# Kernel optimization log

Hardware: AMD Instinct MI355X
Metric: run time of the kernel (lower is better)

## Reference

```python
import jax, jax.numpy as jnp
import numpy as np
from jax import lax

B, N, T, H, E, D, K = 2, 1024, 4096, 256, 2, 2, 9


def angle2vector(a):
    return jnp.stack([jnp.sin(a), jnp.cos(a)], axis=-1)


def setup_inputs() -> dict:
    key = jax.random.key(0)
    ks = jax.random.split(key, 16)
    s = jnp.float32(0.05)
    return {
        "x": jax.random.normal(ks[0], (B, N, T), jnp.float32),
        "z": jax.random.uniform(ks[1], (B, T, E, D), jnp.float32, 0.0, 2.0 * np.pi),
        # encoder: depthwise conv (groups=N) then two 1x1 convs
        "dw_w": jax.random.normal(ks[2], (N, 1, K), jnp.float32) * s,
        "dw_b": jax.random.normal(ks[3], (N,), jnp.float32) * s,
        "w1": jax.random.normal(ks[4], (H, N), jnp.float32) * s,
        "b1": jax.random.normal(ks[5], (H,), jnp.float32) * s,
        "w2": jax.random.normal(ks[6], (H, H), jnp.float32) * s,
        "b2": jax.random.normal(ks[7], (H,), jnp.float32) * s,
        # heads (1x1 convs)
        "wm": jax.random.normal(ks[8], (E * D * 2, H), jnp.float32) * s,
        "bm": jax.random.normal(ks[9], (E * D * 2,), jnp.float32) * s,
        "wv": jax.random.normal(ks[10], (E * D, H), jnp.float32) * s,
        "bv": jax.random.normal(ks[11], (E * D,), jnp.float32) * s,
        # feature basis / readout params
        "receptive_fields": jax.random.uniform(ks[12], (N, E, D), jnp.float32, 0.0, 2.0 * np.pi),
        "ensemble_weights": jax.random.normal(ks[13], (N, E), jnp.float32),
        "final_scale": jax.random.normal(ks[14], (N,), jnp.float32) * s,
        "log_tuning_width": jnp.full((1,), np.log(2.0), jnp.float32),
    }


def reference(x, z, dw_w, dw_b, w1, b1, w2, b2, wm, bm, wv, bv,
              receptive_fields, ensemble_weights, final_scale, log_tuning_width):
    # ---- encoder ----
    # depthwise conv1d, kernel_size=K, padding='same', groups=N
    h = lax.conv_general_dilated(
        x, dw_w, window_strides=(1,), padding="SAME",
        feature_group_count=N, dimension_numbers=("NCH", "OIH", "NCH"))
    h = h + dw_b[None, :, None]
    h = jax.nn.relu(jnp.einsum("hn,bnt->bht", w1, h) + b1[None, :, None])
    h = jax.nn.relu(jnp.einsum("gh,bht->bgt", w2, h) + b2[None, :, None])

    # ---- heads ----
    mu = jnp.einsum("oh,bht->bot", wm, h) + bm[None, :, None]  # [B, E*D*2, T]
    mu = mu.transpose(0, 2, 1).reshape(B, T, E, D, 2)
    logvar = jnp.einsum("oh,bht->bot", wv, h) + bv[None, :, None]  # [B, E*D, T]
    logvar = logvar.transpose(0, 2, 1).reshape(B, T, E, D)
    # normalize encodings onto unit circle
    mu = mu / jnp.sqrt(jnp.sum(mu ** 2, axis=-1, keepdims=True))

    # ---- feature basis ('bump') ----
    zv = angle2vector(z)                     # [B, T, E, D, 2]
    rfv = angle2vector(receptive_fields)     # [N, E, D, 2]
    diff = zv[:, :, None] - rfv[None, None]  # [B, T, N, E, D, 2]
    dist = jnp.sum(diff ** 2, axis=(4, 5))   # [B, T, N, E]
    response = jnp.exp(-dist / jnp.exp(log_tuning_width))  # nonlinearity='exp'

    # ---- ensemble-weighted readout ----
    ew = jax.nn.softmax(ensemble_weights, axis=1)  # [N, E]
    responses = jnp.einsum("btne,ne->btn", response, ew)
    responses = responses * jnp.exp(final_scale)[None, None]
    responses = responses.transpose(0, 2, 1)  # [B, N, T]
    return responses, z, mu, logvar
```

## Files before the change

### kernel.cpp

```cpp
#include <hip/hip_runtime.h>
#include <hip/hip_bf16.h>

#define B_ 2
#define N_ 1024
#define T_ 4096
#define H_ 256
#define ROWS_ 8192

typedef float f32x4 __attribute__((ext_vector_type(4)));
typedef __bf16 bf16x8 __attribute__((ext_vector_type(8)));

__device__ __forceinline__ void gl16(const void* g, void* l) {
  __builtin_amdgcn_global_load_lds(
      (const __attribute__((address_space(1))) void*)g,
      (__attribute__((address_space(3))) void*)l, 16, 0, 0);
}

#define WAITV(N) asm volatile("s_waitcnt vmcnt(" #N ")" ::: "memory")
#define FENCE_ALL() asm volatile("s_waitcnt vmcnt(0) lgkmcnt(0)" ::: "memory")
#define LGKM0() asm volatile("s_waitcnt lgkmcnt(0)" ::: "memory")

__global__ __launch_bounds__(256) void cvt_pack(
    const float* __restrict__ w1, const float* __restrict__ w2,
    __bf16* __restrict__ w1p, __bf16* __restrict__ w2p) {
  const int i = blockIdx.x * 256 + threadIdx.x;
  const float* src;
  __bf16* dst;
  int K, kt, s;
  if (i < 65536) {
    kt = i >> 11; s = i & 2047; src = w1; K = 1024; dst = w1p + (size_t)i * 8;
  } else {
    int j = i - 65536;
    kt = j >> 11; s = j & 2047; src = w2; K = 256; dst = w2p + (size_t)j * 8;
  }
  const int pl = s >> 10;
  const int idx = s & 1023;
  const int g = idx >> 2;
  const int cc = (idx & 3) ^ ((g >> 1) & 3);
  const float* p = src + (size_t)g * K + kt * 32 + cc * 8;
  bf16x8 o;
  #pragma unroll
  for (int e = 0; e < 8; ++e) {
    float v = p[e];
    __bf16 h = (__bf16)v;
    o[e] = pl ? (__bf16)(v - (float)h) : h;
  }
  *(bf16x8*)dst = o;
}

__global__ __launch_bounds__(256) void dwconv_t(
    const float* __restrict__ x, const float* __restrict__ w,
    const float* __restrict__ bias, __bf16* __restrict__ h0h,
    __bf16* __restrict__ h0l) {
  __shared__ float xs[64][76];
  const int tid = threadIdx.x;
  const int t0 = blockIdx.x * 64;
  const int n0 = blockIdx.y * 64;
  const int b = blockIdx.z;
  for (int i = tid; i < 64 * 72; i += 256) {
    int rr = i / 72, cc = i % 72;
    int tt = t0 - 4 + cc;
    xs[rr][cc] = (tt >= 0 && tt < T_) ? x[((size_t)(b * N_ + n0 + rr)) * T_ + tt] : 0.f;
  }
  const int nl = tid & 63;
  const int tg = tid >> 6;
  float wr[9];
  #pragma unroll
  for (int k = 0; k < 9; ++k) wr[k] = w[(n0 + nl) * 9 + k];
  const float bb = bias[n0 + nl];
  __syncthreads();
  float win[24];
  #pragma unroll
  for (int c = 0; c < 6; ++c)
    *(f32x4*)&win[c * 4] = *(const f32x4*)&xs[nl][tg * 16 + c * 4];
  const size_t obase = ((size_t)b * T_ + t0 + tg * 16) * N_ + n0 + nl;
  #pragma unroll
  for (int j = 0; j < 16; ++j) {
    float acc = bb;
    #pragma unroll
    for (int k = 0; k < 9; ++k) acc = fmaf(win[j + k], wr[k], acc);
    __bf16 h = (__bf16)acc;
    h0h[obase + (size_t)j * N_] = h;
    h0l[obase + (size_t)j * N_] = (__bf16)(acc - (float)h);
  }
}

__global__ __launch_bounds__(512) void encoder_fused(
    const __bf16* __restrict__ Ah, const __bf16* __restrict__ Al,
    const __bf16* __restrict__ W1P, const float* __restrict__ b1,
    const __bf16* __restrict__ W2P, const float* __restrict__ b2,
    const float* __restrict__ wm, const float* __restrict__ bm,
    const float* __restrict__ wv, const float* __restrict__ bv,
    float* __restrict__ out_mu, float* __restrict__ out_lv) {
  __shared__ __attribute__((aligned(16))) char smem[126976];
  char* const ASB = smem;
  char* const WSB = smem + 8192;
  char* const H1B = smem + 73728;
  float* const WMV = (float*)(smem + 106496);
  float* const H2S = (float*)(smem + 8192);

  const int tid = threadIdx.x;
  const int row0 = blockIdx.x * 32;
  const int lane = tid & 63;
  const int wid = tid >> 6;
  const int wt = (wid >> 2) * 16;
  const int wg = (wid & 3) * 64;
  const int lr = lane & 15;
  const int ls = lane >> 4;

  if (tid < 256) {
    #pragma unroll
    for (int i = 0; i < 8; ++i) WMV[tid * 20 + i] = wm[i * 256 + tid];
    #pragma unroll
    for (int i = 0; i < 4; ++i) WMV[tid * 20 + 8 + i] = wv[i * 256 + tid];
  }
  float b1g[4], b2g[4];
  #pragma unroll
  for (int ni = 0; ni < 4; ++ni) {
    b1g[ni] = b1[wg + ni * 16 + lr];
    b2g[ni] = b2[wg + ni * 16 + lr];
  }
  FENCE_ALL();

  const int a_pl = tid >> 7;
  const int a_idx = tid & 127;
  const int a_r = a_idx >> 2;
  const int a_c = (a_idx & 3) ^ ((a_r >> 1) & 3);
  const __bf16* a_src = (a_pl ? Al : Ah) + (size_t)(row0 + a_r) * 1024 + a_c * 8;
  char* const a_dst = ASB + a_pl * 2048 + a_idx * 16;

  auto STAGE_A = [&](int buf, int kt) {
    if (tid < 256) gl16(a_src + kt * 32, a_dst + buf * 4096);
  };
  auto STAGE_W = [&](int buf, int kt, const __bf16* WP) {
    const char* src = (const char*)WP + (size_t)kt * 32768 + tid * 16;
    char* dst = WSB + buf * 32768 + tid * 16;
    #pragma unroll
    for (int j = 0; j < 4; ++j) gl16(src + j * 8192, dst + j * 8192);
  };
  auto FR_A = [&](int cur, int pl, int r) {
    return *(const bf16x8*)(ASB + cur * 4096 + pl * 2048 + r * 64 +
                            (ls ^ ((r >> 1) & 3)) * 16);
  };
  auto FR_W = [&](int cur, int pl, int g) {
    return *(const bf16x8*)(WSB + cur * 32768 + pl * 16384 + g * 64 +
                            (ls ^ ((g >> 1) & 3)) * 16);
  };

  f32x4 acc[4];
  #pragma unroll
  for (int i = 0; i < 4; ++i) acc[i] = (f32x4)0.f;

  STAGE_A(0, 0); STAGE_W(0, 0, W1P);
  STAGE_A(1, 1); STAGE_W(1, 1, W1P);
  for (int kt = 0; kt < 32; ++kt) {
    const int cur = kt & 1;
    if (kt < 31) {
      if (tid < 256) WAITV(5); else WAITV(4);
    } else {
      WAITV(0);
    }
    __builtin_amdgcn_s_barrier();
    {
      const int ra = wt + lr;
      bf16x8 ah = FR_A(cur, 0, ra);
      bf16x8 al = FR_A(cur, 1, ra);
      __builtin_amdgcn_s_setprio(1);
      #pragma unroll
      for (int ni = 0; ni < 4; ++ni) {
        const int rw = wg + ni * 16 + lr;
        bf16x8 wh = FR_W(cur, 0, rw);
        bf16x8 wl = FR_W(cur, 1, rw);
        acc[ni] = __builtin_amdgcn_mfma_f32_16x16x32_bf16(ah, wh, acc[ni], 0, 0, 0);
        acc[ni] = __builtin_amdgcn_mfma_f32_16x16x32_bf16(ah, wl, acc[ni], 0, 0, 0);
        acc[ni] = __builtin_amdgcn_mfma_f32_16x16x32_bf16(al, wh, acc[ni], 0, 0, 0);
      }
      __builtin_amdgcn_s_setprio(0);
    }
    LGKM0();
    __builtin_amdgcn_s_barrier();
    if (kt < 30) { STAGE_A(cur, kt + 2); STAGE_W(cur, kt + 2, W1P); }
  }

  #pragma unroll
  for (int ni = 0; ni < 4; ++ni) {
    const int g = wg + ni * 16 + lr;
    const int c = g >> 3;
    #pragma unroll
    for (int reg = 0; reg < 4; ++reg) {
      const int t = wt + ls * 4 + reg;
      float v = fmaxf(acc[ni][reg] + b1g[ni], 0.f);
      __bf16 h = (__bf16)v;
      const int off = t * 512 + ((c ^ (t & 7)) * 16) + (g & 7) * 2;
      *(__bf16*)(H1B + off) = h;
      *(__bf16*)(H1B + 16384 + off) = (__bf16)(v - (float)h);
    }
    acc[ni] = (f32x4)0.f;
  }

  STAGE_W(0, 0, W2P);
  STAGE_W(1, 1, W2P);
  for (int kt = 0; kt < 8; ++kt) {
    const int cur = kt & 1;
    if (kt < 7) WAITV(4); else WAITV(0);
    LGKM0();
    __builtin_amdgcn_s_barrier();
    {
      const int t = wt + lr;
      const int ca = ((kt * 4 + ls) ^ (t & 7)) * 16;
      bf16x8 ah = *(const bf16x8*)(H1B + t * 512 + ca);
      bf16x8 al = *(const bf16x8*)(H1B + 16384 + t * 512 + ca);
      __builtin_amdgcn_s_setprio(1);
      #pragma unroll
      for (int ni = 0; ni < 4; ++ni) {
        const int rw = wg + ni * 16 + lr;
        bf16x8 wh = FR_W(cur, 0, rw);
        bf16x8 wl = FR_W(cur, 1, rw);
        acc[ni] = __builtin_amdgcn_mfma_f32_16x16x32_bf16(ah, wh, acc[ni], 0, 0, 0);
        acc[ni] = __builtin_amdgcn_mfma_f32_16x16x32_bf16(ah, wl, acc[ni], 0, 0, 0);
        acc[ni] = __builtin_amdgcn_mfma_f32_16x16x32_bf16(al, wh, acc[ni], 0, 0, 0);
      }
      __builtin_amdgcn_s_setprio(0);
    }
    LGKM0();
    __builtin_amdgcn_s_barrier();
    if (kt < 6) STAGE_W(cur, kt + 2, W2P);
  }

  #pragma unroll
  for (int ni = 0; ni < 4; ++ni) {
    const int g = wg + ni * 16 + lr;
    #pragma unroll
    for (int reg = 0; reg < 4; ++reg) {
      const int t = wt + ls * 4 + reg;
      H2S[t * 264 + g] = fmaxf(acc[ni][reg] + b2g[ni], 0.f);
    }
  }
  LGKM0();
  __builtin_amdgcn_s_barrier();

  const int ht = tid >> 4;
  const int sub = tid & 15;
  float s[12];
  #pragma unroll
  for (int o = 0; o < 12; ++o) s[o] = 0.f;
  #pragma unroll
  for (int j = 0; j < 16; ++j) {
    const int k = sub + j * 16;
    const float hv = H2S[ht * 264 + k];
    const float* wp = &WMV[k * 20];
    #pragma unroll
    for (int o = 0; o < 12; ++o) s[o] = fmaf(wp[o], hv, s[o]);
  }
  #pragma unroll
  for (int o = 0; o < 12; ++o) {
    s[o] += __shfl_xor(s[o], 1);
    s[o] += __shfl_xor(s[o], 2);
    s[o] += __shfl_xor(s[o], 4);
    s[o] += __shfl_xor(s[o], 8);
  }
  const size_t row = row0 + ht;
  if (sub == 0) {
    float mm[8];
    #pragma unroll
    for (int ed = 0; ed < 4; ++ed) {
      float m0 = s[ed * 2] + bm[ed * 2];
      float m1 = s[ed * 2 + 1] + bm[ed * 2 + 1];
      float inv = 1.f / sqrtf(m0 * m0 + m1 * m1);
      mm[ed * 2] = m0 * inv;
      mm[ed * 2 + 1] = m1 * inv;
    }
    *(float4*)&out_mu[row * 8] = make_float4(mm[0], mm[1], mm[2], mm[3]);
    *(float4*)&out_mu[row * 8 + 4] = make_float4(mm[4], mm[5], mm[6], mm[7]);
  } else if (sub == 1) {
    *(float4*)&out_lv[row * 4] =
        make_float4(s[8] + bv[0], s[9] + bv[1], s[10] + bv[2], s[11] + bv[3]);
  }
}

__global__ __launch_bounds__(256) void resp_kernel(
    const float* __restrict__ z, const float* __restrict__ rf,
    const float* __restrict__ ew, const float* __restrict__ fs,
    const float* __restrict__ ltw, float* __restrict__ out,
    float* __restrict__ out_z) {
  __shared__ float s_sin[32][4], s_cos[32][4], s_w[32][2];
  const int tid = threadIdx.x;
  const int tc = blockIdx.x;
  const int nc = blockIdx.y;
  const int b = blockIdx.z;
  if (tid < 128) {
    int nl = tid >> 2, ed = tid & 3;
    float a = rf[(nc * 32 + nl) * 4 + ed];
    s_sin[nl][ed] = sinf(a);
    s_cos[nl][ed] = cosf(a);
  }
  if (tid < 32) {
    int n = nc * 32 + tid;
    float e0 = ew[n * 2], e1 = ew[n * 2 + 1];
    float m = fmaxf(e0, e1);
    float x0 = expf(e0 - m), x1 = expf(e1 - m);
    float sc = expf(fs[n]) / (x0 + x1);
    s_w[tid][0] = x0 * sc;
    s_w[tid][1] = x1 * sc;
  }
  __syncthreads();
  const int t = tc * 1024 + (tid >> 6) * 256 + (tid & 63) * 4;
  const float inv_tw = expf(-ltw[0]);
  float sz[16], cz[16];
  #pragma unroll
  for (int j = 0; j < 4; ++j) {
    float4 zv = *(const float4*)&z[((size_t)b * T_ + t + j) * 4];
    if (nc == 0) *(float4*)&out_z[((size_t)b * T_ + t + j) * 4] = zv;
    sz[j * 4 + 0] = sinf(zv.x); cz[j * 4 + 0] = cosf(zv.x);
    sz[j * 4 + 1] = sinf(zv.y); cz[j * 4 + 1] = cosf(zv.y);
    sz[j * 4 + 2] = sinf(zv.z); cz[j * 4 + 2] = cosf(zv.z);
    sz[j * 4 + 3] = sinf(zv.w); cz[j * 4 + 3] = cosf(zv.w);
  }
  float* op = out + (size_t)b * N_ * T_ + (size_t)(nc * 32) * T_ + t;
  for (int nl = 0; nl < 32; ++nl) {
    const float ss0 = s_sin[nl][0], sc0 = s_cos[nl][0];
    const float ss1 = s_sin[nl][1], sc1 = s_cos[nl][1];
    const float ss2 = s_sin[nl][2], sc2 = s_cos[nl][2];
    const float ss3 = s_sin[nl][3], sc3 = s_cos[nl][3];
    const float w0 = s_w[nl][0], w1 = s_w[nl][1];
    float o[4];
    #pragma unroll
    for (int j = 0; j < 4; ++j) {
      float d0 = sz[j * 4] * ss0 + cz[j * 4] * sc0 + sz[j * 4 + 1] * ss1 + cz[j * 4 + 1] * sc1;
      float d1 = sz[j * 4 + 2] * ss2 + cz[j * 4 + 2] * sc2 + sz[j * 4 + 3] * ss3 + cz[j * 4 + 3] * sc3;
      float r0 = __expf((2.f * d0 - 4.f) * inv_tw);
      float r1 = __expf((2.f * d1 - 4.f) * inv_tw);
      o[j] = w0 * r0 + w1 * r1;
    }
    *(float4*)&op[(size_t)nl * T_] = make_float4(o[0], o[1], o[2], o[3]);
  }
}

extern "C" void kernel_launch(void* const* d_in, const int* in_sizes, int n_in,
                              void* d_out, int out_size, void* d_ws, size_t ws_size,
                              hipStream_t stream) {
  const float* x   = (const float*)d_in[0];
  const float* z   = (const float*)d_in[1];
  const float* dww = (const float*)d_in[2];
  const float* dwb = (const float*)d_in[3];
  const float* w1  = (const float*)d_in[4];
  const float* b1  = (const float*)d_in[5];
  const float* w2  = (const float*)d_in[6];
  const float* b2  = (const float*)d_in[7];
  const float* wm  = (const float*)d_in[8];
  const float* bm  = (const float*)d_in[9];
  const float* wv  = (const float*)d_in[10];
  const float* bv  = (const float*)d_in[11];
  const float* rf  = (const float*)d_in[12];
  const float* ew  = (const float*)d_in[13];
  const float* fs  = (const float*)d_in[14];
  const float* ltw = (const float*)d_in[15];

  float* out = (float*)d_out;
  float* out_resp = out;
  float* out_z    = out + (size_t)B_ * N_ * T_;
  float* out_mu   = out_z + (size_t)B_ * T_ * 4;
  float* out_lv   = out_mu + (size_t)B_ * T_ * 8;

  __bf16* h0h = (__bf16*)out_resp;
  __bf16* h0l = h0h + (size_t)ROWS_ * N_;

  __bf16* p = (__bf16*)d_ws;
  __bf16* w1p = p; p += 524288;
  __bf16* w2p = p; p += 131072;

  cvt_pack<<<320, 256, 0, stream>>>(w1, w2, w1p, w2p);
  dwconv_t<<<dim3(T_ / 64, N_ / 64, B_), 256, 0, stream>>>(x, dww, dwb, h0h, h0l);
  encoder_fused<<<dim3(ROWS_ / 32), 512, 0, stream>>>(
      h0h, h0l, w1p, b1, w2p, b2, wm, bm, wv, bv, out_mu, out_lv);
  resp_kernel<<<dim3(4, 32, 2), 256, 0, stream>>>(
      z, rf, ew, fs, ltw, out_resp, out_z);
}
```

Measured before the change: 175.8 us.

## Merge encoder and response kernels into one launch with larger row tiles

Fuses the encoder GEMM kernel and the response kernel into one launch: the first 128 blocks run the encoder, the remaining 128 blocks compute responses. Each encoder block now handles 64 rows, doubling the reuse of the staged weights, and the bf16 intermediate moves from the response output buffer into workspace so both parts can run at the same time. In exchange, shared memory per block grows and the encoder has fewer blocks to spread across the CUs.

```diff
diff --git a/kernel.cpp b/kernel.cpp
--- a/kernel.cpp
+++ b/kernel.cpp
@@ -6,6 +6,7 @@
 #define T_ 4096
 #define H_ 256
 #define ROWS_ 8192
+#define ENC_BLOCKS 128
 
 typedef float f32x4 __attribute__((ext_vector_type(4)));
 typedef __bf16 bf16x8 __attribute__((ext_vector_type(8)));
@@ -85,34 +86,96 @@
   }
 }
 
-__global__ __launch_bounds__(512) void encoder_fused(
+__global__ __launch_bounds__(512) void mega_kernel(
     const __bf16* __restrict__ Ah, const __bf16* __restrict__ Al,
     const __bf16* __restrict__ W1P, const float* __restrict__ b1,
     const __bf16* __restrict__ W2P, const float* __restrict__ b2,
     const float* __restrict__ wm, const float* __restrict__ bm,
     const float* __restrict__ wv, const float* __restrict__ bv,
-    float* __restrict__ out_mu, float* __restrict__ out_lv) {
-  __shared__ __attribute__((aligned(16))) char smem[126976];
+    float* __restrict__ out_mu, float* __restrict__ out_lv,
+    const float* __restrict__ z, const float* __restrict__ rf,
+    const float* __restrict__ ew, const float* __restrict__ fs,
+    const float* __restrict__ ltw, float* __restrict__ out_resp,
+    float* __restrict__ out_z) {
+  __shared__ __attribute__((aligned(16))) char smem[159744];
+  const int tid = threadIdx.x;
+
+  if (blockIdx.x >= ENC_BLOCKS) {
+    float* s_sin = (float*)smem;
+    float* s_cos = (float*)(smem + 512);
+    float* s_w   = (float*)(smem + 1024);
+    const int bid2 = blockIdx.x - ENC_BLOCKS;
+    const int nc = bid2 & 31;
+    const int tc = (bid2 >> 5) & 1;
+    const int b = bid2 >> 6;
+    if (tid < 128) {
+      int nl = tid >> 2, ed = tid & 3;
+      float a = rf[(nc * 32 + nl) * 4 + ed];
+      s_sin[nl * 4 + ed] = sinf(a);
+      s_cos[nl * 4 + ed] = cosf(a);
+    }
+    if (tid < 32) {
+      int n = nc * 32 + tid;
+      float e0 = ew[n * 2], e1 = ew[n * 2 + 1];
+      float m = fmaxf(e0, e1);
+      float x0 = expf(e0 - m), x1 = expf(e1 - m);
+      float sc = expf(fs[n]) / (x0 + x1);
+      s_w[tid * 2 + 0] = x0 * sc;
+      s_w[tid * 2 + 1] = x1 * sc;
+    }
+    __syncthreads();
+    const int t = tc * 2048 + tid * 4;
+    const float inv_tw = expf(-ltw[0]);
+    float sz[16], cz[16];
+    #pragma unroll
+    for (int j = 0; j < 4; ++j) {
+      float4 zv = *(const float4*)&z[((size_t)b * T_ + t + j) * 4];
+      if (nc == 0) *(float4*)&out_z[((size_t)b * T_ + t + j) * 4] = zv;
+      sz[j * 4 + 0] = sinf(zv.x); cz[j * 4 + 0] = cosf(zv.x);
+      sz[j * 4 + 1] = sinf(zv.y); cz[j * 4 + 1] = cosf(zv.y);
+      sz[j * 4 + 2] = sinf(zv.z); cz[j * 4 + 2] = cosf(zv.z);
+      sz[j * 4 + 3] = sinf(zv.w); cz[j * 4 + 3] = cosf(zv.w);
+    }
+    float* op = out_resp + (size_t)b * N_ * T_ + (size_t)(nc * 32) * T_ + t;
+    for (int nl = 0; nl < 32; ++nl) {
+      const float ss0 = s_sin[nl * 4 + 0], sc0 = s_cos[nl * 4 + 0];
+      const float ss1 = s_sin[nl * 4 + 1], sc1 = s_cos[nl * 4 + 1];
+      const float ss2 = s_sin[nl * 4 + 2], sc2 = s_cos[nl * 4 + 2];
+      const float ss3 = s_sin[nl * 4 + 3], sc3 = s_cos[nl * 4 + 3];
+      const float w0 = s_w[nl * 2 + 0], w1 = s_w[nl * 2 + 1];
+      float o[4];
+      #pragma unroll
+      for (int j = 0; j < 4; ++j) {
+        float d0 = sz[j * 4] * ss0 + cz[j * 4] * sc0 + sz[j * 4 + 1] * ss1 + cz[j * 4 + 1] * sc1;
+        float d1 = sz[j * 4 + 2] * ss2 + cz[j * 4 + 2] * sc2 + sz[j * 4 + 3] * ss3 + cz[j * 4 + 3] * sc3;
+        float r0 = __expf((2.f * d0 - 4.f) * inv_tw);
+        float r1 = __expf((2.f * d1 - 4.f) * inv_tw);
+        o[j] = w0 * r0 + w1 * r1;
+      }
+      *(float4*)&op[(size_t)nl * T_] = make_float4(o[0], o[1], o[2], o[3]);
+    }
+    return;
+  }
+
   char* const ASB = smem;
-  char* const WSB = smem + 8192;
-  char* const H1B = smem + 73728;
-  float* const WMV = (float*)(smem + 106496);
-  float* const H2S = (float*)(smem + 8192);
-
-  const int tid = threadIdx.x;
-  const int row0 = blockIdx.x * 32;
+  char* const WSB = smem + 16384;
+  char* const H1B = smem + 81920;
+  float* const WMV = (float*)(smem + 147456);
+  float* const H2S = (float*)smem;
+
+  const int row0 = blockIdx.x * 64;
   const int lane = tid & 63;
   const int wid = tid >> 6;
-  const int wt = (wid >> 2) * 16;
+  const int wt = (wid >> 2) * 32;
   const int wg = (wid & 3) * 64;
   const int lr = lane & 15;
   const int ls = lane >> 4;
 
   if (tid < 256) {
     #pragma unroll
-    for (int i = 0; i < 8; ++i) WMV[tid * 20 + i] = wm[i * 256 + tid];
-    #pragma unroll
-    for (int i = 0; i < 4; ++i) WMV[tid * 20 + 8 + i] = wv[i * 256 + tid];
+    for (int i = 0; i < 8; ++i) WMV[tid * 12 + i] = wm[i * 256 + tid];
+    #pragma unroll
+    for (int i = 0; i < 4; ++i) WMV[tid * 12 + 8 + i] = wv[i * 256 + tid];
   }
   float b1g[4], b2g[4];
   #pragma unroll
@@ -122,15 +185,15 @@
   }
   FENCE_ALL();
 
-  const int a_pl = tid >> 7;
-  const int a_idx = tid & 127;
+  const int a_pl = tid >> 8;
+  const int a_idx = tid & 255;
   const int a_r = a_idx >> 2;
   const int a_c = (a_idx & 3) ^ ((a_r >> 1) & 3);
   const __bf16* a_src = (a_pl ? Al : Ah) + (size_t)(row0 + a_r) * 1024 + a_c * 8;
-  char* const a_dst = ASB + a_pl * 2048 + a_idx * 16;
+  char* const a_dst = ASB + a_pl * 4096 + a_idx * 16;
 
   auto STAGE_A = [&](int buf, int kt) {
-    if (tid < 256) gl16(a_src + kt * 32, a_dst + buf * 4096);
+    gl16(a_src + kt * 32, a_dst + buf * 8192);
   };
   auto STAGE_W = [&](int buf, int kt, const __bf16* WP) {
     const char* src = (const char*)WP + (size_t)kt * 32768 + tid * 16;
@@ -139,7 +202,7 @@
     for (int j = 0; j < 4; ++j) gl16(src + j * 8192, dst + j * 8192);
   };
   auto FR_A = [&](int cur, int pl, int r) {
-    return *(const bf16x8*)(ASB + cur * 4096 + pl * 2048 + r * 64 +
+    return *(const bf16x8*)(ASB + cur * 8192 + pl * 4096 + r * 64 +
                             (ls ^ ((r >> 1) & 3)) * 16);
   };
   auto FR_W = [&](int cur, int pl, int g) {
@@ -147,33 +210,37 @@
                             (ls ^ ((g >> 1) & 3)) * 16);
   };
 
-  f32x4 acc[4];
-  #pragma unroll
-  for (int i = 0; i < 4; ++i) acc[i] = (f32x4)0.f;
+  f32x4 acc[2][4];
+  #pragma unroll
+  for (int i = 0; i < 2; ++i)
+    #pragma unroll
+    for (int j = 0; j < 4; ++j) acc[i][j] = (f32x4)0.f;
 
   STAGE_A(0, 0); STAGE_W(0, 0, W1P);
   STAGE_A(1, 1); STAGE_W(1, 1, W1P);
   for (int kt = 0; kt < 32; ++kt) {
     const int cur = kt & 1;
-    if (kt < 31) {
-      if (tid < 256) WAITV(5); else WAITV(4);
-    } else {
-      WAITV(0);
-    }
+    if (kt < 31) WAITV(5); else WAITV(0);
     __builtin_amdgcn_s_barrier();
     {
-      const int ra = wt + lr;
-      bf16x8 ah = FR_A(cur, 0, ra);
-      bf16x8 al = FR_A(cur, 1, ra);
+      bf16x8 ah[2], al[2];
+      #pragma unroll
+      for (int mi = 0; mi < 2; ++mi) {
+        ah[mi] = FR_A(cur, 0, wt + mi * 16 + lr);
+        al[mi] = FR_A(cur, 1, wt + mi * 16 + lr);
+      }
       __builtin_amdgcn_s_setprio(1);
       #pragma unroll
       for (int ni = 0; ni < 4; ++ni) {
         const int rw = wg + ni * 16 + lr;
         bf16x8 wh = FR_W(cur, 0, rw);
         bf16x8 wl = FR_W(cur, 1, rw);
-        acc[ni] = __builtin_amdgcn_mfma_f32_16x16x32_bf16(ah, wh, acc[ni], 0, 0, 0);
-        acc[ni] = __builtin_amdgcn_mfma_f32_16x16x32_bf16(ah, wl, acc[ni], 0, 0, 0);
-        acc[ni] = __builtin_amdgcn_mfma_f32_16x16x32_bf16(al, wh, acc[ni], 0, 0, 0);
+        #pragma unroll
+        for (int mi = 0; mi < 2; ++mi) {
+          acc[mi][ni] = __builtin_amdgcn_mfma_f32_16x16x32_bf16(ah[mi], wh, acc[mi][ni], 0, 0, 0);
+          acc[mi][ni] = __builtin_amdgcn_mfma_f32_16x16x32_bf16(ah[mi], wl, acc[mi][ni], 0, 0, 0);
+          acc[mi][ni] = __builtin_amdgcn_mfma_f32_16x16x32_bf16(al[mi], wh, acc[mi][ni], 0, 0, 0);
+        }
       }
       __builtin_amdgcn_s_setprio(0);
     }
@@ -183,20 +250,22 @@
   }
 
   #pragma unroll
-  for (int ni = 0; ni < 4; ++ni) {
-    const int g = wg + ni * 16 + lr;
-    const int c = g >> 3;
-    #pragma unroll
-    for (int reg = 0; reg < 4; ++reg) {
-      const int t = wt + ls * 4 + reg;
-      float v = fmaxf(acc[ni][reg] + b1g[ni], 0.f);
-      __bf16 h = (__bf16)v;
-      const int off = t * 512 + ((c ^ (t & 7)) * 16) + (g & 7) * 2;
-      *(__bf16*)(H1B + off) = h;
-      *(__bf16*)(H1B + 16384 + off) = (__bf16)(v - (float)h);
-    }
-    acc[ni] = (f32x4)0.f;
-  }
+  for (int mi = 0; mi < 2; ++mi)
+    #pragma unroll
+    for (int ni = 0; ni < 4; ++ni) {
+      const int g = wg + ni * 16 + lr;
+      const int c = g >> 3;
+      #pragma unroll
+      for (int reg = 0; reg < 4; ++reg) {
+        const int t = wt + mi * 16 + ls * 4 + reg;
+        float v = fmaxf(acc[mi][ni][reg] + b1g[ni], 0.f);
+        __bf16 h = (__bf16)v;
+        const int off = t * 512 + ((c ^ (t & 7)) * 16) + (g & 7) * 2;
+        *(__bf16*)(H1B + off) = h;
+        *(__bf16*)(H1B + 32768 + off) = (__bf16)(v - (float)h);
+      }
+      acc[mi][ni] = (f32x4)0.f;
+    }
 
   STAGE_W(0, 0, W2P);
   STAGE_W(1, 1, W2P);
@@ -206,19 +275,26 @@
     LGKM0();
     __builtin_amdgcn_s_barrier();
     {
-      const int t = wt + lr;
-      const int ca = ((kt * 4 + ls) ^ (t & 7)) * 16;
-      bf16x8 ah = *(const bf16x8*)(H1B + t * 512 + ca);
-      bf16x8 al = *(const bf16x8*)(H1B + 16384 + t * 512 + ca);
+      bf16x8 ah[2], al[2];
+      #pragma unroll
+      for (int mi = 0; mi < 2; ++mi) {
+        const int t = wt + mi * 16 + lr;
+        const int ca = ((kt * 4 + ls) ^ (t & 7)) * 16;
+        ah[mi] = *(const bf16x8*)(H1B + t * 512 + ca);
+        al[mi] = *(const bf16x8*)(H1B + 32768 + t * 512 + ca);
+      }
       __builtin_amdgcn_s_setprio(1);
       #pragma unroll
       for (int ni = 0; ni < 4; ++ni) {
         const int rw = wg + ni * 16 + lr;
         bf16x8 wh = FR_W(cur, 0, rw);
         bf16x8 wl = FR_W(cur, 1, rw);
-        acc[ni] = __builtin_amdgcn_mfma_f32_16x16x32_bf16(ah, wh, acc[ni], 0, 0, 0);
-        acc[ni] = __builtin_amdgcn_mfma_f32_16x16x32_bf16(ah, wl, acc[ni], 0, 0, 0);
-        acc[ni] = __builtin_amdgcn_mfma_f32_16x16x32_bf16(al, wh, acc[ni], 0, 0, 0);
+        #pragma unroll
+        for (int mi = 0; mi < 2; ++mi) {
+          acc[mi][ni] = __builtin_amdgcn_mfma_f32_16x16x32_bf16(ah[mi], wh, acc[mi][ni], 0, 0, 0);
+          acc[mi][ni] = __builtin_amdgcn_mfma_f32_16x16x32_bf16(ah[mi], wl, acc[mi][ni], 0, 0, 0);
+          acc[mi][ni] = __builtin_amdgcn_mfma_f32_16x16x32_bf16(al[mi], wh, acc[mi][ni], 0, 0, 0);
+        }
       }
       __builtin_amdgcn_s_setprio(0);
     }
@@ -228,27 +304,29 @@
   }
 
   #pragma unroll
-  for (int ni = 0; ni < 4; ++ni) {
-    const int g = wg + ni * 16 + lr;
-    #pragma unroll
-    for (int reg = 0; reg < 4; ++reg) {
-      const int t = wt + ls * 4 + reg;
-      H2S[t * 264 + g] = fmaxf(acc[ni][reg] + b2g[ni], 0.f);
-    }
-  }
+  for (int mi = 0; mi < 2; ++mi)
+    #pragma unroll
+    for (int ni = 0; ni < 4; ++ni) {
+      const int g = wg + ni * 16 + lr;
+      #pragma unroll
+      for (int reg = 0; reg < 4; ++reg) {
+        const int t = wt + mi * 16 + ls * 4 + reg;
+        H2S[t * 257 + g] = fmaxf(acc[mi][ni][reg] + b2g[ni], 0.f);
+      }
+    }
   LGKM0();
   __builtin_amdgcn_s_barrier();
 
-  const int ht = tid >> 4;
-  const int sub = tid & 15;
+  const int ht = tid >> 3;
+  const int sub = tid & 7;
   float s[12];
   #pragma unroll
   for (int o = 0; o < 12; ++o) s[o] = 0.f;
   #pragma unroll
-  for (int j = 0; j < 16; ++j) {
-    const int k = sub + j * 16;
-    const float hv = H2S[ht * 264 + k];
-    const float* wp = &WMV[k * 20];
+  for (int j = 0; j < 32; ++j) {
+    const int k = sub + j * 8;
+    const float hv = H2S[ht * 257 + k];
+    const float* wp = &WMV[k * 12];
     #pragma unroll
     for (int o = 0; o < 12; ++o) s[o] = fmaf(wp[o], hv, s[o]);
   }
@@ -257,7 +335,6 @@
     s[o] += __shfl_xor(s[o], 1);
     s[o] += __shfl_xor(s[o], 2);
     s[o] += __shfl_xor(s[o], 4);
-    s[o] += __shfl_xor(s[o], 8);
   }
   const size_t row = row0 + ht;
   if (sub == 0) {
@@ -275,64 +352,6 @@
   } else if (sub == 1) {
     *(float4*)&out_lv[row * 4] =
         make_float4(s[8] + bv[0], s[9] + bv[1], s[10] + bv[2], s[11] + bv[3]);
-  }
-}
-
-__global__ __launch_bounds__(256) void resp_kernel(
-    const float* __restrict__ z, const float* __restrict__ rf,
-    const float* __restrict__ ew, const float* __restrict__ fs,
-    const float* __restrict__ ltw, float* __restrict__ out,
-    float* __restrict__ out_z) {
-  __shared__ float s_sin[32][4], s_cos[32][4], s_w[32][2];
-  const int tid = threadIdx.x;
-  const int tc = blockIdx.x;
-  const int nc = blockIdx.y;
-  const int b = blockIdx.z;
-  if (tid < 128) {
-    int nl = tid >> 2, ed = tid & 3;
-    float a = rf[(nc * 32 + nl) * 4 + ed];
-    s_sin[nl][ed] = sinf(a);
-    s_cos[nl][ed] = cosf(a);
-  }
-  if (tid < 32) {
-    int n = nc * 32 + tid;
-    float e0 = ew[n * 2], e1 = ew[n * 2 + 1];
-    float m = fmaxf(e0, e1);
-    float x0 = expf(e0 - m), x1 = expf(e1 - m);
-    float sc = expf(fs[n]) / (x0 + x1);
-    s_w[tid][0] = x0 * sc;
-    s_w[tid][1] = x1 * sc;
-  }
-  __syncthreads();
-  const int t = tc * 1024 + (tid >> 6) * 256 + (tid & 63) * 4;
-  const float inv_tw = expf(-ltw[0]);
-  float sz[16], cz[16];
-  #pragma unroll
-  for (int j = 0; j < 4; ++j) {
-    float4 zv = *(const float4*)&z[((size_t)b * T_ + t + j) * 4];
-    if (nc == 0) *(float4*)&out_z[((size_t)b * T_ + t + j) * 4] = zv;
-    sz[j * 4 + 0] = sinf(zv.x); cz[j * 4 + 0] = cosf(zv.x);
-    sz[j * 4 + 1] = sinf(zv.y); cz[j * 4 + 1] = cosf(zv.y);
-    sz[j * 4 + 2] = sinf(zv.z); cz[j * 4 + 2] = cosf(zv.z);
-    sz[j * 4 + 3] = sinf(zv.w); cz[j * 4 + 3] = cosf(zv.w);
-  }
-  float* op = out + (size_t)b * N_ * T_ + (size_t)(nc * 32) * T_ + t;
-  for (int nl = 0; nl < 32; ++nl) {
-    const float ss0 = s_sin[nl][0], sc0 = s_cos[nl][0];
-    const float ss1 = s_sin[nl][1], sc1 = s_cos[nl][1];
-    const float ss2 = s_sin[nl][2], sc2 = s_cos[nl][2];
-    const float ss3 = s_sin[nl][3], sc3 = s_cos[nl][3];
-    const float w0 = s_w[nl][0], w1 = s_w[nl][1];
-    float o[4];
-    #pragma unroll
-    for (int j = 0; j < 4; ++j) {
-      float d0 = sz[j * 4] * ss0 + cz[j * 4] * sc0 + sz[j * 4 + 1] * ss1 + cz[j * 4 + 1] * sc1;
-      float d1 = sz[j * 4 + 2] * ss2 + cz[j * 4 + 2] * sc2 + sz[j * 4 + 3] * ss3 + cz[j * 4 + 3] * sc3;
-      float r0 = __expf((2.f * d0 - 4.f) * inv_tw);
-      float r1 = __expf((2.f * d1 - 4.f) * inv_tw);
-      o[j] = w0 * r0 + w1 * r1;
-    }
-    *(float4*)&op[(size_t)nl * T_] = make_float4(o[0], o[1], o[2], o[3]);
   }
 }
 
@@ -362,17 +381,15 @@
   float* out_mu   = out_z + (size_t)B_ * T_ * 4;
   float* out_lv   = out_mu + (size_t)B_ * T_ * 8;
 
-  __bf16* h0h = (__bf16*)out_resp;
-  __bf16* h0l = h0h + (size_t)ROWS_ * N_;
-
   __bf16* p = (__bf16*)d_ws;
   __bf16* w1p = p; p += 524288;
   __bf16* w2p = p; p += 131072;
+  __bf16* h0h = p; p += (size_t)ROWS_ * N_;
+  __bf16* h0l = p; p += (size_t)ROWS_ * N_;
 
   cvt_pack<<<320, 256, 0, stream>>>(w1, w2, w1p, w2p);
   dwconv_t<<<dim3(T_ / 64, N_ / 64, B_), 256, 0, stream>>>(x, dww, dwb, h0h, h0l);
-  encoder_fused<<<dim3(ROWS_ / 32), 512, 0, stream>>>(
-      h0h, h0l, w1p, b1, w2p, b2, wm, bm, wv, bv, out_mu, out_lv);
-  resp_kernel<<<dim3(4, 32, 2), 256, 0, stream>>>(
+  mega_kernel<<<dim3(256), 512, 0, stream>>>(
+      h0h, h0l, w1p, b1, w2p, b2, wm, bm, wv, bv, out_mu, out_lv,
       z, rf, ew, fs, ltw, out_resp, out_z);
 }
```

Result: faster. 163.6 us (-7.0%).
